# Kernel optimization log

Measured on AMD Instinct MI355X. Metric: run time of the kernel, lower is better.

## Reference

```python
import jax, jax.numpy as jnp
import numpy as np

N = 50000          # num nodes
NUM_HE = 10000     # num hyperedges
E = 800000         # num graph edges
INC = 800000       # num (node, hyperedge) incidences
IN_C, HID, OUT_C = 128, 128, 64
SLOPE = 0.01       # torch leaky_relu default negative slope


def _leaky(x):
    return jnp.where(x >= 0, x, SLOPE * x)


def hypergraph_conv(x, he_index, theta, bias):
    # PyG HypergraphConv (no attention, unit hyperedge weights):
    # out = D^{-1} H B^{-1} H^T (X Theta) + bias
    node_idx, he_idx = he_index[0], he_index[1]
    x = x @ theta                                            # [N, F]
    ones = jnp.ones(node_idx.shape[0], x.dtype)
    D = jax.ops.segment_sum(ones, node_idx, num_segments=N)           # node degree
    B = jax.ops.segment_sum(ones, he_idx, num_segments=NUM_HE)        # hyperedge degree
    Dinv = jnp.where(D > 0, 1.0 / D, 0.0)
    Binv = jnp.where(B > 0, 1.0 / B, 0.0)
    # node -> hyperedge
    m = jax.ops.segment_sum(x[node_idx], he_idx, num_segments=NUM_HE) * Binv[:, None]
    # hyperedge -> node
    out = jax.ops.segment_sum(m[he_idx], node_idx, num_segments=N) * Dinv[:, None]
    return out + bias


def graph_conv(x, edge_index, w_rel, b_rel, w_root):
    # PyG GraphConv (aggr='add'): out_i = W_rel * sum_{j->i} x_j + b_rel + W_root * x_i
    src, dst = edge_index[0], edge_index[1]
    agg = jax.ops.segment_sum(x[src], dst, num_segments=N)
    return agg @ w_rel + b_rel + x @ w_root


def _forward(X, edge_index, hyperedge_index,
             hc1_w, hc1_b, lin1_w, lin1_b,
             hc2_w, hc2_b, lin2_w, lin2_b,
             c1_wrel, c1_brel, c1_wroot, glin1_w, glin1_b,
             c2_wrel, c2_brel, c2_wroot, glin2_w, glin2_b,
             fc_w, fc_b):
    # dropout is identity in eval mode (and first two calls in the source discard their output)
    X = _leaky(hypergraph_conv(X, hyperedge_index, hc1_w, hc1_b) + (X @ lin1_w + lin1_b))
    X = _leaky(hypergraph_conv(X, hyperedge_index, hc2_w, hc2_b) + (X @ lin2_w + lin2_b))
    X = _leaky(graph_conv(X, edge_index, c1_wrel, c1_brel, c1_wroot) + (X @ glin1_w + glin1_b))
    X = _leaky(graph_conv(X, edge_index, c2_wrel, c2_brel, c2_wroot) + (X @ glin2_w + glin2_b))
    y = X @ fc_w + fc_b
    return X, y


def setup_inputs() -> dict:
    key = jax.random.key(0)
    ks = jax.random.split(key, 32)
    s = 0.02
    inp = {
        'X': jax.random.normal(ks[0], (N, IN_C), jnp.float32),
        'edge_index': jnp.stack([
            jax.random.randint(ks[1], (E,), 0, N),
            jax.random.randint(ks[2], (E,), 0, N)]).astype(jnp.int64),
        'hyperedge_index': jnp.stack([
            jax.random.randint(ks[3], (INC,), 0, N),
            jax.random.randint(ks[4], (INC,), 0, NUM_HE)]).astype(jnp.int64),
        'hc1_w': jax.random.normal(ks[5], (IN_C, HID), jnp.float32) * s,
        'hc1_b': jnp.zeros((HID,), jnp.float32),
        'lin1_w': jax.random.normal(ks[6], (IN_C, HID), jnp.float32) * s,
        'lin1_b': jnp.zeros((HID,), jnp.float32),
        'hc2_w': jax.random.normal(ks[7], (HID, HID), jnp.float32) * s,
        'hc2_b': jnp.zeros((HID,), jnp.float32),
        'lin2_w': jax.random.normal(ks[8], (HID, HID), jnp.float32) * s,
        'lin2_b': jnp.zeros((HID,), jnp.float32),
        'c1_wrel': jax.random.normal(ks[9], (HID, HID), jnp.float32) * s,
        'c1_brel': jnp.zeros((HID,), jnp.float32),
        'c1_wroot': jax.random.normal(ks[10], (HID, HID), jnp.float32) * s,
        'glin1_w': jax.random.normal(ks[11], (HID, HID), jnp.float32) * s,
        'glin1_b': jnp.zeros((HID,), jnp.float32),
        'c2_wrel': jax.random.normal(ks[12], (HID, HID), jnp.float32) * s,
        'c2_brel': jnp.zeros((HID,), jnp.float32),
        'c2_wroot': jax.random.normal(ks[13], (HID, HID), jnp.float32) * s,
        'glin2_w': jax.random.normal(ks[14], (HID, HID), jnp.float32) * s,
        'glin2_b': jnp.zeros((HID,), jnp.float32),
        'fc_w': jax.random.normal(ks[15], (HID, OUT_C), jnp.float32) * s,
        'fc_b': jnp.zeros((OUT_C,), jnp.float32),
    }
    return inp


def reference(X, edge_index, hyperedge_index,
              hc1_w, hc1_b, lin1_w, lin1_b,
              hc2_w, hc2_b, lin2_w, lin2_b,
              c1_wrel, c1_brel, c1_wroot, glin1_w, glin1_b,
              c2_wrel, c2_brel, c2_wroot, glin2_w, glin2_b,
              fc_w, fc_b):
    return _forward(X, edge_index, hyperedge_index,
                    hc1_w, hc1_b, lin1_w, lin1_b,
                    hc2_w, hc2_b, lin2_w, lin2_b,
                    c1_wrel, c1_brel, c1_wroot, glin1_w, glin1_b,
                    c2_wrel, c2_brel, c2_wroot, glin2_w, glin2_b,
                    fc_w, fc_b)
```

## Files before the change

### kernel.cpp

```cpp
#include <hip/hip_runtime.h>

#define NN 50000
#define HECNT 10000
#define EE 800000
#define II 800000
#define NBK 128
#define CHUNK 4096
#define BKCAP 8192

typedef _Float16 half8 __attribute__((ext_vector_type(8)));
typedef float f32x4    __attribute__((ext_vector_type(4)));
typedef unsigned short u16;

__device__ __forceinline__ int ld_idx(const int* p, long long pos, int is64) {
    return is64 ? p[pos * 2] : p[(int)pos];
}

__device__ __forceinline__ void task_info(int t, int& n, int& cbase, int& obase) {
    if (t == 0)      { n = HECNT; cbase = 0;           obase = 0; }
    else if (t == 1) { n = NN;    cbase = HECNT;       obase = HECNT + 1; }
    else             { n = NN;    cbase = HECNT + NN;  obase = HECNT + NN + 2; }
}

__device__ __forceinline__ void ld_edge(int t, long long i,
                                        const int* EIX, const int* HIX,
                                        int f0, int f1, int& d, int& v) {
    int rng;
    if (t == 0)      { d = ld_idx(HIX, (long long)II + i, f1); v = ld_idx(HIX, i, f1); rng = HECNT; }
    else if (t == 1) { d = ld_idx(HIX, i, f1); v = ld_idx(HIX, (long long)II + i, f1); rng = NN; }
    else             { d = ld_idx(EIX, (long long)EE + i, f0); v = ld_idx(EIX, i, f0); rng = NN; }
    if ((unsigned)d >= (unsigned)rng || (unsigned)v >= 65536u) d = -1;
}

__global__ void detect_binit_k(const int* __restrict__ EIX, const int* __restrict__ HIX,
                               int* __restrict__ flags, int* __restrict__ bcur) {
    int tid = threadIdx.x;
    int i = blockIdx.x * 256 + tid;
    if (i < 3 * NBK) bcur[i] = i * BKCAP;
    if (blockIdx.x == 0) {
        __shared__ int o0, o1;
        if (tid == 0) { o0 = 0; o1 = 0; }
        __syncthreads();
        atomicOr(&o0, EIX[2 * tid + 1]);
        atomicOr(&o1, HIX[2 * tid + 1]);
        __syncthreads();
        if (tid == 0) { flags[0] = (o0 == 0); flags[1] = (o1 == 0); }
    }
}

__global__ __launch_bounds__(256) void bin_k(const int* __restrict__ EIX,
                                             const int* __restrict__ HIX,
                                             const int* __restrict__ flags,
                                             int* __restrict__ bcur,
                                             unsigned* __restrict__ pairs) {
    int t = blockIdx.y;
    __shared__ int hcnt[NBK], hstart[NBK], hrun[NBK], gbase[NBK];
    __shared__ int stot;
    __shared__ unsigned stage[CHUNK];
    int tid = threadIdx.x;
    int n, cb, ob; task_info(t, n, cb, ob);
    int span = (n + NBK - 1) / NBK;
    long long base = (long long)blockIdx.x * CHUNK;
    int f0 = flags[0], f1 = flags[1];

    for (int i = tid; i < NBK; i += 256) { hcnt[i] = 0; hrun[i] = 0; }
    __syncthreads();

    int d[16], v[16];
    #pragma unroll
    for (int j = 0; j < 16; j++) {
        long long i = base + j * 256 + tid;
        int dd = -1, vv = 0;
        if (i < EE) ld_edge(t, i, EIX, HIX, f0, f1, dd, vv);
        d[j] = dd; v[j] = vv;
        if (dd >= 0) atomicAdd(&hcnt[dd / span], 1);
    }
    __syncthreads();

    if (tid < NBK) gbase[tid] = hcnt[tid] ? atomicAdd(&bcur[t * NBK + tid], hcnt[tid]) : 0;
    if (tid < NBK) hstart[tid] = hcnt[tid];
    __syncthreads();
    for (int o = 1; o < NBK; o <<= 1) {
        int u = 0;
        if (tid < NBK && tid >= o) u = hstart[tid - o];
        __syncthreads();
        if (tid < NBK) hstart[tid] += u;
        __syncthreads();
    }
    if (tid == NBK - 1) stot = hstart[tid];
    __syncthreads();
    if (tid < NBK) hstart[tid] -= hcnt[tid];
    __syncthreads();

    #pragma unroll
    for (int j = 0; j < 16; j++) {
        if (d[j] >= 0) {
            int b = d[j] / span;
            int p = hstart[b] + atomicAdd(&hrun[b], 1);
            stage[p] = ((unsigned)d[j] << 16) | (unsigned)v[j];
        }
    }
    __syncthreads();

    int total = stot;
    for (int i = tid; i < total; i += 256) {
        int lo = 0, hi = NBK - 1;
        while (lo < hi) { int mid = (lo + hi + 1) >> 1; if (hstart[mid] <= i) lo = mid; else hi = mid - 1; }
        int pos = gbase[lo] + (i - hstart[lo]);
        if (pos < (t * NBK + lo + 1) * BKCAP)
            pairs[pos] = stage[lo == 0 ? i : i];
    }
}

__global__ __launch_bounds__(384) void bscan_k(const int* __restrict__ bcur,
                                               int* __restrict__ bbase,
                                               int* __restrict__ offs) {
    __shared__ int sc[3 * NBK];
    int tid = threadIdx.x;
    int c = 0;
    if (tid < 3 * NBK) {
        c = bcur[tid] - tid * BKCAP;
        c = max(0, min(c, BKCAP));
        sc[tid] = c;
    }
    __syncthreads();
    int b = tid & (NBK - 1);
    for (int o = 1; o < NBK; o <<= 1) {
        int u = 0;
        if (tid < 3 * NBK && b >= o) u = sc[tid - o];
        __syncthreads();
        if (tid < 3 * NBK) sc[tid] += u;
        __syncthreads();
    }
    if (tid < 3 * NBK) {
        bbase[tid] = sc[tid] - c;
        if (b == NBK - 1) {
            int t = tid >> 7;
            int n, cb, ob; task_info(t, n, cb, ob);
            offs[ob + n] = sc[tid];
        }
    }
}

__global__ __launch_bounds__(256) void bfin_k(const int* __restrict__ bcur,
                                              const int* __restrict__ bbase,
                                              const unsigned* __restrict__ pairs,
                                              int* __restrict__ offs,
                                              u16* __restrict__ vals) {
    int idx = blockIdx.x;
    int t = idx / NBK, b = idx % NBK;
    int n, cb, ob; task_info(t, n, cb, ob);
    int span = (n + NBK - 1) / NBK;
    int dlo = min(b * span, n), dhi = min(dlo + span, n);
    if (dhi <= dlo) return;
    int nd = dhi - dlo;
    int cnt = bcur[idx] - idx * BKCAP;
    cnt = max(0, min(cnt, BKCAP));
    int base = bbase[idx];

    __shared__ int hist[512], sc[512], cur[400];
    __shared__ u16 win[BKCAP];
    int tid = threadIdx.x;
    for (int i = tid; i < 512; i += 256) { hist[i] = 0; }
    __syncthreads();

    const unsigned* pw = pairs + (size_t)idx * BKCAP;
    for (int i = tid; i < cnt; i += 256) {
        int dl = (int)(pw[i] >> 16) - dlo;
        if ((unsigned)dl < (unsigned)nd) atomicAdd(&hist[dl], 1);
    }
    __syncthreads();

    int s0 = tid, s1 = tid + 256;
    sc[s0] = hist[s0]; sc[s1] = hist[s1];
    __syncthreads();
    for (int o = 1; o < 512; o <<= 1) {
        int u0 = (s0 >= o) ? sc[s0 - o] : 0;
        int u1 = (s1 >= o) ? sc[s1 - o] : 0;
        __syncthreads();
        sc[s0] += u0; sc[s1] += u1;
        __syncthreads();
    }
    for (int i = tid; i < nd; i += 256) {
        int ex = sc[i] - hist[i];
        offs[ob + dlo + i] = base + ex;
        cur[i] = ex;
    }
    __syncthreads();

    for (int i = tid; i < cnt; i += 256) {
        unsigned pv = pw[i];
        int dl = (int)(pv >> 16) - dlo;
        if ((unsigned)dl < (unsigned)nd) {
            int p = atomicAdd(&cur[dl], 1);
            if ((unsigned)p < (unsigned)BKCAP) win[p] = (u16)(pv & 0xffffu);
        }
    }
    __syncthreads();
    u16* vw = vals + (size_t)t * 800000 + base;
    for (int i = tid; i < cnt; i += 256) vw[i] = win[i];
}

__global__ __launch_bounds__(256) void gather_k(const int* __restrict__ offs,
                                                const u16* __restrict__ vals,
                                                const _Float16* __restrict__ src,
                                                _Float16* __restrict__ out,
                                                int ndst, int nsrc, int scale_flag,
                                                const float* __restrict__ bias,
                                                const _Float16* __restrict__ addend,
                                                int act) {
    int wave = threadIdx.x >> 6, lane = threadIdx.x & 63;
    int sub = lane >> 4, l16 = lane & 15;
    int d = blockIdx.x * 4 + wave;
    if (d >= ndst) return;
    int beg = offs[d], end = offs[d + 1];
    int f = l16 * 8;
    float a[8] = {0.f, 0.f, 0.f, 0.f, 0.f, 0.f, 0.f, 0.f};
    auto acc_row = [&](int s) {
        if ((unsigned)s < (unsigned)nsrc) {
            half8 u = *(const half8*)(src + (size_t)s * 128 + f);
            #pragma unroll
            for (int j = 0; j < 8; j++) a[j] += (float)u[j];
        }
    };
    int e = beg + sub;
    for (; e + 12 < end; e += 16) {
        int s0 = vals[e], s1 = vals[e + 4], s2 = vals[e + 8], s3 = vals[e + 12];
        acc_row(s0); acc_row(s1); acc_row(s2); acc_row(s3);
    }
    for (; e < end; e += 4) acc_row(vals[e]);
    #pragma unroll
    for (int j = 0; j < 8; j++) {
        a[j] += __shfl_xor(a[j], 16, 64);
        a[j] += __shfl_xor(a[j], 32, 64);
    }
    if (sub == 0) {
        if (scale_flag) {
            int c = end - beg;
            float iv = (c > 0) ? 1.f / (float)c : 0.f;
            #pragma unroll
            for (int j = 0; j < 8; j++) a[j] *= iv;
        }
        if (bias) {
            f32x4 b0 = *(const f32x4*)(bias + f);
            f32x4 b1 = *(const f32x4*)(bias + f + 4);
            #pragma unroll
            for (int j = 0; j < 4; j++) { a[j] += b0[j]; a[4 + j] += b1[j]; }
        }
        if (addend) {
            half8 u = *(const half8*)(addend + (size_t)d * 128 + f);
            #pragma unroll
            for (int j = 0; j < 8; j++) a[j] += (float)u[j];
        }
        if (act) {
            #pragma unroll
            for (int j = 0; j < 8; j++) a[j] = (a[j] >= 0.f) ? a[j] : 0.01f * a[j];
        }
        half8 o;
        #pragma unroll
        for (int j = 0; j < 8; j++) o[j] = (_Float16)a[j];
        *(half8*)(out + (size_t)d * 128 + f) = o;
    }
}

__global__ __launch_bounds__(256) void wprep_k(const float* __restrict__ hc1_w, const float* __restrict__ lin1_w,
                                               const float* __restrict__ hc2_w, const float* __restrict__ lin2_w,
                                               const float* __restrict__ c1_wrel, const float* __restrict__ c1_wroot,
                                               const float* __restrict__ glin1_w,
                                               const float* __restrict__ c2_wrel, const float* __restrict__ c2_wroot,
                                               const float* __restrict__ glin2_w,
                                               const float* __restrict__ fc_w,
                                               _Float16* __restrict__ F) {
    int set = blockIdx.y;
    int nfrag = (set == 4) ? 1024 : 4096;
    int NT = (set < 2) ? 16 : (set == 4 ? 4 : 8);
    int fid = blockIdx.x * 256 + threadIdx.x;
    if (fid >= nfrag) return;
    int lane = fid & 63;
    int tile = fid >> 6;
    int nt = tile % NT, ks = tile / NT;
    int n = nt * 16 + (lane & 15);
    int kbase = ks * 32 + (lane >> 4) * 8;
    _Float16* dst = F + (size_t)set * 32768 + (size_t)fid * 8;
    #pragma unroll
    for (int j = 0; j < 8; j++) {
        int k = kbase + j;
        float w;
        if (set == 0)      w = (n < 128) ? hc1_w[k * 128 + n] : lin1_w[k * 128 + n - 128];
        else if (set == 1) w = (n < 128) ? hc2_w[k * 128 + n] : lin2_w[k * 128 + n - 128];
        else if (set == 2) w = (k < 128) ? c1_wrel[k * 128 + n]
                                         : c1_wroot[(k - 128) * 128 + n] + glin1_w[(k - 128) * 128 + n];
        else if (set == 3) w = (k < 128) ? c2_wrel[k * 128 + n]
                                         : c2_wroot[(k - 128) * 128 + n] + glin2_w[(k - 128) * 128 + n];
        else               w = fc_w[k * 64 + n];
        dst[j] = (_Float16)w;
    }
}

template <typename AT>
__global__ __launch_bounds__(256) void gemm2_k(const AT* __restrict__ A,
                                               const half8* __restrict__ Bf,
                                               const float* __restrict__ b2,
                                               _Float16* __restrict__ O1,
                                               _Float16* __restrict__ O2,
                                               int M) {
    constexpr int K = 128, NT = 16;
    int tid = threadIdx.x;
    int wave = tid >> 6, lane = tid & 63;
    int quad = lane >> 4, l16 = lane & 15;
    int rowbase = blockIdx.x * 64 + wave * 16;
    int row = rowbase + l16;

    f32x4 acc[NT];
    f32x4 zero4 = {0.f, 0.f, 0.f, 0.f};
    #pragma unroll
    for (int nt = 0; nt < NT; nt++) acc[nt] = zero4;

    #pragma unroll
    for (int ks = 0; ks < 4; ks++) {
        int k0 = ks * 32 + quad * 8;
        half8 af = {0, 0, 0, 0, 0, 0, 0, 0};
        if (row < M) {
            if constexpr (sizeof(AT) == 4) {
                const float* ap = (const float*)A + (size_t)row * K + k0;
                float4 x0 = *(const float4*)ap;
                float4 x1 = *(const float4*)(ap + 4);
                af = half8{(_Float16)x0.x, (_Float16)x0.y, (_Float16)x0.z, (_Float16)x0.w,
                           (_Float16)x1.x, (_Float16)x1.y, (_Float16)x1.z, (_Float16)x1.w};
            } else {
                af = *(const half8*)((const _Float16*)A + (size_t)row * K + k0);
            }
        }
        #pragma unroll
        for (int nt = 0; nt < NT; nt++) {
            half8 bfr = Bf[(ks * NT + nt) * 64 + lane];
            acc[nt] = __builtin_amdgcn_mfma_f32_16x16x32_f16(af, bfr, acc[nt], 0, 0, 0);
        }
    }

    #pragma unroll
    for (int nt = 0; nt < NT; nt++) {
        int col = nt * 16 + l16;
        bool second = (col >= 128);
        int c = second ? col - 128 : col;
        float bv = second ? b2[c] : 0.f;
        _Float16* O = second ? O2 : O1;
        #pragma unroll
        for (int r = 0; r < 4; r++) {
            int rr = rowbase + quad * 4 + r;
            if (rr < M) O[(size_t)rr * 128 + c] = (_Float16)(acc[nt][r] + bv);
        }
    }
}

__global__ __launch_bounds__(256) void gemmk2_k(const _Float16* __restrict__ A0,
                                                const _Float16* A1,
                                                const half8* __restrict__ Bf,
                                                const float* __restrict__ brel,
                                                const float* __restrict__ blin,
                                                float* __restrict__ Cf,
                                                _Float16* Ch,
                                                int M) {
    constexpr int NT = 8;
    int tid = threadIdx.x;
    int wave = tid >> 6, lane = tid & 63;
    int quad = lane >> 4, l16 = lane & 15;
    int rowbase = blockIdx.x * 64 + wave * 16;
    int row = rowbase + l16;

    f32x4 acc[NT];
    f32x4 zero4 = {0.f, 0.f, 0.f, 0.f};
    #pragma unroll
    for (int nt = 0; nt < NT; nt++) acc[nt] = zero4;

    #pragma unroll
    for (int ks = 0; ks < 8; ks++) {
        int k0 = ks * 32 + quad * 8;
        const _Float16* Asel = (k0 < 128) ? A0 : A1;
        int ka = k0 & 127;
        half8 af = {0, 0, 0, 0, 0, 0, 0, 0};
        if (row < M) af = *(const half8*)(Asel + (size_t)row * 128 + ka);
        #pragma unroll
        for (int nt = 0; nt < NT; nt++) {
            half8 bfr = Bf[(ks * NT + nt) * 64 + lane];
            acc[nt] = __builtin_amdgcn_mfma_f32_16x16x32_f16(af, bfr, acc[nt], 0, 0, 0);
        }
    }

    #pragma unroll
    for (int nt = 0; nt < NT; nt++) {
        int col = nt * 16 + l16;
        float bv = brel[col] + blin[col];
        #pragma unroll
        for (int r = 0; r < 4; r++) {
            int rr = rowbase + quad * 4 + r;
            if (rr < M) {
                float v = acc[nt][r] + bv;
                v = (v >= 0.f) ? v : 0.01f * v;
                if (Cf) Cf[(size_t)rr * 128 + col] = v;
                Ch[(size_t)rr * 128 + col] = (_Float16)v;
            }
        }
    }
}

__global__ __launch_bounds__(256) void gemmfc_k(const _Float16* __restrict__ A,
                                                const half8* __restrict__ Bf,
                                                const float* __restrict__ bias,
                                                float* __restrict__ C,
                                                int M) {
    constexpr int K = 128, N = 64, NT = 4;
    int tid = threadIdx.x;
    int wave = tid >> 6, lane = tid & 63;
    int quad = lane >> 4, l16 = lane & 15;
    int rowbase = blockIdx.x * 64 + wave * 16;
    int row = rowbase + l16;

    f32x4 acc[NT];
    f32x4 zero4 = {0.f, 0.f, 0.f, 0.f};
    #pragma unroll
    for (int nt = 0; nt < NT; nt++) acc[nt] = zero4;

    #pragma unroll
    for (int ks = 0; ks < 4; ks++) {
        int k0 = ks * 32 + quad * 8;
        half8 af = {0, 0, 0, 0, 0, 0, 0, 0};
        if (row < M) af = *(const half8*)(A + (size_t)row * K + k0);
        #pragma unroll
        for (int nt = 0; nt < NT; nt++) {
            half8 bfr = Bf[(ks * NT + nt) * 64 + lane];
            acc[nt] = __builtin_amdgcn_mfma_f32_16x16x32_f16(af, bfr, acc[nt], 0, 0, 0);
        }
    }

    #pragma unroll
    for (int nt = 0; nt < NT; nt++) {
        int col = nt * 16 + l16;
        float bv = bias[col];
        #pragma unroll
        for (int r = 0; r < 4; r++) {
            int rr = rowbase + quad * 4 + r;
            if (rr < M) C[(size_t)rr * N + col] = acc[nt][r] + bv;
        }
    }
}

extern "C" void kernel_launch(void* const* d_in, const int* in_sizes, int n_in,
                              void* d_out, int out_size, void* d_ws, size_t ws_size,
                              hipStream_t stream) {
    const float* X       = (const float*)d_in[0];
    const int*   EIX     = (const int*)d_in[1];
    const int*   HIX     = (const int*)d_in[2];
    const float* hc1_w   = (const float*)d_in[3];
    const float* hc1_b   = (const float*)d_in[4];
    const float* lin1_w  = (const float*)d_in[5];
    const float* lin1_b  = (const float*)d_in[6];
    const float* hc2_w   = (const float*)d_in[7];
    const float* hc2_b   = (const float*)d_in[8];
    const float* lin2_w  = (const float*)d_in[9];
    const float* lin2_b  = (const float*)d_in[10];
    const float* c1_wrel = (const float*)d_in[11];
    const float* c1_brel = (const float*)d_in[12];
    const float* c1_wroot= (const float*)d_in[13];
    const float* glin1_w = (const float*)d_in[14];
    const float* glin1_b = (const float*)d_in[15];
    const float* c2_wrel = (const float*)d_in[16];
    const float* c2_brel = (const float*)d_in[17];
    const float* c2_wroot= (const float*)d_in[18];
    const float* glin2_w = (const float*)d_in[19];
    const float* glin2_b = (const float*)d_in[20];
    const float* fc_w    = (const float*)d_in[21];
    const float* fc_b    = (const float*)d_in[22];

    char* wsp = (char*)d_ws;
    size_t off = 0;
    auto carve = [&](size_t bytes) -> char* {
        char* p = wsp + off;
        off = (off + bytes + 255) & ~(size_t)255;
        return p;
    };
    int*   flags  = (int*)carve(16);
    int*   offs   = (int*)carve(110003 * 4);
    int*   bcur   = (int*)carve(3 * NBK * 4);
    int*   bbase  = (int*)carve(3 * NBK * 4);
    u16*   vals   = (u16*)carve(2400000 * 2);
    _Float16* F   = (_Float16*)carve((4 * 32768 + 8192) * 2);
    char*  U      = carve((size_t)NN * 128 * 2 * 2);
    _Float16* P  = (_Float16*)U;
    _Float16* L  = (_Float16*)(U + (size_t)NN * 128 * 2);
    unsigned* pairs = (unsigned*)U;
    _Float16* MH = (_Float16*)carve((size_t)HECNT * 128 * 2);
    _Float16* XA = (_Float16*)carve((size_t)NN * 128 * 2);

    float* XO = (float*)d_out;
    float* YO = XO + (size_t)NN * 128;

    const half8* F0 = (const half8*)F;
    const half8* F1 = (const half8*)(F + 32768);
    const half8* F2 = (const half8*)(F + 2 * 32768);
    const half8* F3 = (const half8*)(F + 3 * 32768);
    const half8* F4 = (const half8*)(F + 4 * 32768);

    detect_binit_k<<<2, 256, 0, stream>>>(EIX, HIX, flags, bcur);
    wprep_k<<<dim3(16, 5), 256, 0, stream>>>(hc1_w, lin1_w, hc2_w, lin2_w,
                                             c1_wrel, c1_wroot, glin1_w,
                                             c2_wrel, c2_wroot, glin2_w, fc_w, F);
    bin_k<<<dim3((EE + CHUNK - 1) / CHUNK, 3), 256, 0, stream>>>(EIX, HIX, flags, bcur, pairs);
    bscan_k<<<1, 384, 0, stream>>>(bcur, bbase, offs);
    bfin_k<<<3 * NBK, 256, 0, stream>>>(bcur, bbase, pairs, offs, vals);

    const int* offs_he   = offs;
    const int* offs_node = offs + HECNT + 1;
    const int* offs_dst  = offs + HECNT + NN + 2;
    const u16* vals_he   = vals;
    const u16* vals_node = vals + 800000;
    const u16* vals_dst  = vals + 1600000;

    int g64 = (NN + 63) / 64;
    int ghe = (HECNT + 3) / 4;
    int gnn = (NN + 3) / 4;

    gemm2_k<float><<<g64, 256, 0, stream>>>(X, F0, lin1_b, P, L, NN);
    gather_k<<<ghe, 256, 0, stream>>>(offs_he, vals_he, P, MH, HECNT, NN, 1, nullptr, nullptr, 0);
    gather_k<<<gnn, 256, 0, stream>>>(offs_node, vals_node, MH, XA, NN, HECNT, 1, hc1_b, L, 1);

    gemm2_k<_Float16><<<g64, 256, 0, stream>>>(XA, F1, lin2_b, P, L, NN);
    gather_k<<<ghe, 256, 0, stream>>>(offs_he, vals_he, P, MH, HECNT, NN, 1, nullptr, nullptr, 0);
    gather_k<<<gnn, 256, 0, stream>>>(offs_node, vals_node, MH, XA, NN, HECNT, 1, hc2_b, L, 1);

    gather_k<<<gnn, 256, 0, stream>>>(offs_dst, vals_dst, XA, P, NN, NN, 0, nullptr, nullptr, 0);
    gemmk2_k<<<g64, 256, 0, stream>>>(P, XA, F2, c1_brel, glin1_b, nullptr, XA, NN);

    gather_k<<<gnn, 256, 0, stream>>>(offs_dst, vals_dst, XA, P, NN, NN, 0, nullptr, nullptr, 0);
    gemmk2_k<<<g64, 256, 0, stream>>>(P, XA, F3, c2_brel, glin2_b, XO, XA, NN);

    gemmfc_k<<<g64, 256, 0, stream>>>(XA, F4, fc_b, YO, NN);
}
```

Measured before the change: 477.2 us.

## Fuse preprocessing, binning with first GEMM, and gathers into GEMM kernels

Merges the flag/bucket init into the weight-prep kernel, runs edge binning and the first projection GEMM in one launch, and folds the bucket scan into the finalize kernel. Gathers feeding GEMMs now write into LDS tiles consumed directly by MFMA, and the final FC GEMM is fused into the last graph-conv kernel. Binning loads are vectorized and the gather loop is unrolled deeper. This cuts launch count and intermediate HBM round-trips, but per-block gather work in the fused kernels is serialized over 16 rows per wave, which may lower parallelism.

Result: slower. 531.2 us (+11.3%).

```diff
diff --git a/kernel.cpp b/kernel.cpp
--- a/kernel.cpp
+++ b/kernel.cpp
@@ -7,14 +7,11 @@
 #define NBK 128
 #define CHUNK 4096
 #define BKCAP 8192
+#define BIN_GRID ((EE + CHUNK - 1) / CHUNK)
 
 typedef _Float16 half8 __attribute__((ext_vector_type(8)));
 typedef float f32x4    __attribute__((ext_vector_type(4)));
 typedef unsigned short u16;
-
-__device__ __forceinline__ int ld_idx(const int* p, long long pos, int is64) {
-    return is64 ? p[pos * 2] : p[(int)pos];
-}
 
 __device__ __forceinline__ void task_info(int t, int& n, int& cbase, int& obase) {
     if (t == 0)      { n = HECNT; cbase = 0;           obase = 0; }
@@ -22,22 +19,21 @@
     else             { n = NN;    cbase = HECNT + NN;  obase = HECNT + NN + 2; }
 }
 
-__device__ __forceinline__ void ld_edge(int t, long long i,
-                                        const int* EIX, const int* HIX,
-                                        int f0, int f1, int& d, int& v) {
-    int rng;
-    if (t == 0)      { d = ld_idx(HIX, (long long)II + i, f1); v = ld_idx(HIX, i, f1); rng = HECNT; }
-    else if (t == 1) { d = ld_idx(HIX, i, f1); v = ld_idx(HIX, (long long)II + i, f1); rng = NN; }
-    else             { d = ld_idx(EIX, (long long)EE + i, f0); v = ld_idx(EIX, i, f0); rng = NN; }
-    if ((unsigned)d >= (unsigned)rng || (unsigned)v >= 65536u) d = -1;
-}
-
-__global__ void detect_binit_k(const int* __restrict__ EIX, const int* __restrict__ HIX,
-                               int* __restrict__ flags, int* __restrict__ bcur) {
+__global__ __launch_bounds__(256) void prep_k(const int* __restrict__ EIX, const int* __restrict__ HIX,
+                                              int* __restrict__ flags, int* __restrict__ bcur,
+                                              const float* __restrict__ hc1_w, const float* __restrict__ lin1_w,
+                                              const float* __restrict__ hc2_w, const float* __restrict__ lin2_w,
+                                              const float* __restrict__ c1_wrel, const float* __restrict__ c1_wroot,
+                                              const float* __restrict__ glin1_w,
+                                              const float* __restrict__ c2_wrel, const float* __restrict__ c2_wroot,
+                                              const float* __restrict__ glin2_w,
+                                              const float* __restrict__ fc_w,
+                                              _Float16* __restrict__ F) {
+    int set = blockIdx.y;
     int tid = threadIdx.x;
-    int i = blockIdx.x * 256 + tid;
-    if (i < 3 * NBK) bcur[i] = i * BKCAP;
-    if (blockIdx.x == 0) {
+    if (set == 5) {
+        if (blockIdx.x != 0) return;
+        for (int i = tid; i < 3 * NBK; i += 256) bcur[i] = i * BKCAP;
         __shared__ int o0, o1;
         if (tid == 0) { o0 = 0; o1 = 0; }
         __syncthreads();
@@ -45,35 +41,77 @@
         atomicOr(&o1, HIX[2 * tid + 1]);
         __syncthreads();
         if (tid == 0) { flags[0] = (o0 == 0); flags[1] = (o1 == 0); }
-    }
-}
-
-__global__ __launch_bounds__(256) void bin_k(const int* __restrict__ EIX,
-                                             const int* __restrict__ HIX,
-                                             const int* __restrict__ flags,
-                                             int* __restrict__ bcur,
-                                             unsigned* __restrict__ pairs) {
-    int t = blockIdx.y;
+        return;
+    }
+    int nfrag = (set == 4) ? 1024 : 4096;
+    int NT = (set < 2) ? 16 : (set == 4 ? 4 : 8);
+    int fid = blockIdx.x * 256 + tid;
+    if (fid >= nfrag) return;
+    int lane = fid & 63;
+    int tile = fid >> 6;
+    int nt = tile % NT, ks = tile / NT;
+    int n = nt * 16 + (lane & 15);
+    int kbase = ks * 32 + (lane >> 4) * 8;
+    _Float16* dst = F + (size_t)set * 32768 + (size_t)fid * 8;
+    #pragma unroll
+    for (int j = 0; j < 8; j++) {
+        int k = kbase + j;
+        float w;
+        if (set == 0)      w = (n < 128) ? hc1_w[k * 128 + n] : lin1_w[k * 128 + n - 128];
+        else if (set == 1) w = (n < 128) ? hc2_w[k * 128 + n] : lin2_w[k * 128 + n - 128];
+        else if (set == 2) w = (k < 128) ? c1_wrel[k * 128 + n]
+                                         : c1_wroot[(k - 128) * 128 + n] + glin1_w[(k - 128) * 128 + n];
+        else if (set == 3) w = (k < 128) ? c2_wrel[k * 128 + n]
+                                         : c2_wroot[(k - 128) * 128 + n] + glin2_w[(k - 128) * 128 + n];
+        else               w = fc_w[k * 64 + n];
+        dst[j] = (_Float16)w;
+    }
+}
+
+__device__ void bin_body(int bx, int t,
+                         const int* __restrict__ EIX, const int* __restrict__ HIX,
+                         const int* __restrict__ flags, int* __restrict__ bcur,
+                         unsigned* __restrict__ pairs) {
     __shared__ int hcnt[NBK], hstart[NBK], hrun[NBK], gbase[NBK];
     __shared__ int stot;
     __shared__ unsigned stage[CHUNK];
     int tid = threadIdx.x;
     int n, cb, ob; task_info(t, n, cb, ob);
     int span = (n + NBK - 1) / NBK;
-    long long base = (long long)blockIdx.x * CHUNK;
-    int f0 = flags[0], f1 = flags[1];
+    long long base = (long long)bx * CHUNK;
+    int f = (t == 2) ? flags[0] : flags[1];
+    const int* arr = (t == 2) ? EIX : HIX;
+    int mul = f ? 2 : 1;
+    const int* row1 = arr + (size_t)mul * 800000;
+    const int* darr = (t == 1) ? arr : row1;
+    const int* varr = (t == 1) ? row1 : arr;
+    int rng = (t == 0) ? HECNT : NN;
 
     for (int i = tid; i < NBK; i += 256) { hcnt[i] = 0; hrun[i] = 0; }
     __syncthreads();
 
     int d[16], v[16];
     #pragma unroll
-    for (int j = 0; j < 16; j++) {
-        long long i = base + j * 256 + tid;
-        int dd = -1, vv = 0;
-        if (i < EE) ld_edge(t, i, EIX, HIX, f0, f1, dd, vv);
-        d[j] = dd; v[j] = vv;
-        if (dd >= 0) atomicAdd(&hcnt[dd / span], 1);
+    for (int jj = 0; jj < 8; jj++) {
+        long long i = base + jj * 512 + tid * 2;
+        int d0 = -1, d1 = -1, v0 = 0, v1 = 0;
+        if (i < EE) {
+            if (f) {
+                int4 dw = *(const int4*)(darr + 2 * i);
+                int4 vw = *(const int4*)(varr + 2 * i);
+                d0 = dw.x; d1 = dw.z; v0 = vw.x; v1 = vw.z;
+            } else {
+                int2 dw = *(const int2*)(darr + i);
+                int2 vw = *(const int2*)(varr + i);
+                d0 = dw.x; d1 = dw.y; v0 = vw.x; v1 = vw.y;
+            }
+            if ((unsigned)d0 >= (unsigned)rng || (unsigned)v0 >= 65536u) d0 = -1;
+            if ((unsigned)d1 >= (unsigned)rng || (unsigned)v1 >= 65536u) d1 = -1;
+        }
+        d[2 * jj] = d0; v[2 * jj] = v0;
+        d[2 * jj + 1] = d1; v[2 * jj + 1] = v1;
+        if (d0 >= 0) atomicAdd(&hcnt[d0 / span], 1);
+        if (d1 >= 0) atomicAdd(&hcnt[d1 / span], 1);
     }
     __syncthreads();
 
@@ -108,59 +146,105 @@
         while (lo < hi) { int mid = (lo + hi + 1) >> 1; if (hstart[mid] <= i) lo = mid; else hi = mid - 1; }
         int pos = gbase[lo] + (i - hstart[lo]);
         if (pos < (t * NBK + lo + 1) * BKCAP)
-            pairs[pos] = stage[lo == 0 ? i : i];
-    }
-}
-
-__global__ __launch_bounds__(384) void bscan_k(const int* __restrict__ bcur,
-                                               int* __restrict__ bbase,
-                                               int* __restrict__ offs) {
-    __shared__ int sc[3 * NBK];
+            pairs[pos] = stage[i];
+    }
+}
+
+__device__ void gemm2_f32(int bx, const float* __restrict__ A,
+                          const half8* __restrict__ Bf,
+                          const float* __restrict__ b2,
+                          _Float16* __restrict__ O1, _Float16* __restrict__ O2, int M) {
+    constexpr int K = 128, NT = 16;
     int tid = threadIdx.x;
-    int c = 0;
-    if (tid < 3 * NBK) {
-        c = bcur[tid] - tid * BKCAP;
-        c = max(0, min(c, BKCAP));
-        sc[tid] = c;
-    }
-    __syncthreads();
-    int b = tid & (NBK - 1);
-    for (int o = 1; o < NBK; o <<= 1) {
-        int u = 0;
-        if (tid < 3 * NBK && b >= o) u = sc[tid - o];
-        __syncthreads();
-        if (tid < 3 * NBK) sc[tid] += u;
-        __syncthreads();
-    }
-    if (tid < 3 * NBK) {
-        bbase[tid] = sc[tid] - c;
-        if (b == NBK - 1) {
-            int t = tid >> 7;
-            int n, cb, ob; task_info(t, n, cb, ob);
-            offs[ob + n] = sc[tid];
-        }
-    }
-}
-
-__global__ __launch_bounds__(256) void bfin_k(const int* __restrict__ bcur,
-                                              const int* __restrict__ bbase,
-                                              const unsigned* __restrict__ pairs,
-                                              int* __restrict__ offs,
-                                              u16* __restrict__ vals) {
+    int wave = tid >> 6, lane = tid & 63;
+    int quad = lane >> 4, l16 = lane & 15;
+    int rowbase = bx * 64 + wave * 16;
+    int row = rowbase + l16;
+
+    f32x4 acc[NT];
+    f32x4 zero4 = {0.f, 0.f, 0.f, 0.f};
+    #pragma unroll
+    for (int nt = 0; nt < NT; nt++) acc[nt] = zero4;
+
+    #pragma unroll
+    for (int ks = 0; ks < 4; ks++) {
+        int k0 = ks * 32 + quad * 8;
+        half8 af = {0, 0, 0, 0, 0, 0, 0, 0};
+        if (row < M) {
+            const float* ap = A + (size_t)row * K + k0;
+            float4 x0 = *(const float4*)ap;
+            float4 x1 = *(const float4*)(ap + 4);
+            af = half8{(_Float16)x0.x, (_Float16)x0.y, (_Float16)x0.z, (_Float16)x0.w,
+                       (_Float16)x1.x, (_Float16)x1.y, (_Float16)x1.z, (_Float16)x1.w};
+        }
+        #pragma unroll
+        for (int nt = 0; nt < NT; nt++) {
+            half8 bfr = Bf[(ks * NT + nt) * 64 + lane];
+            acc[nt] = __builtin_amdgcn_mfma_f32_16x16x32_f16(af, bfr, acc[nt], 0, 0, 0);
+        }
+    }
+
+    #pragma unroll
+    for (int nt = 0; nt < NT; nt++) {
+        int col = nt * 16 + l16;
+        bool second = (col >= 128);
+        int c = second ? col - 128 : col;
+        float bv = second ? b2[c] : 0.f;
+        _Float16* O = second ? O2 : O1;
+        #pragma unroll
+        for (int r = 0; r < 4; r++) {
+            int rr = rowbase + quad * 4 + r;
+            if (rr < M) O[(size_t)rr * 128 + c] = (_Float16)(acc[nt][r] + bv);
+        }
+    }
+}
+
+__global__ __launch_bounds__(256) void phase1_k(const int* __restrict__ EIX, const int* __restrict__ HIX,
+                                                const int* __restrict__ flags, int* __restrict__ bcur,
+                                                unsigned* __restrict__ pairs,
+                                                const float* __restrict__ X, const half8* __restrict__ F0,
+                                                const float* __restrict__ lin1_b,
+                                                _Float16* __restrict__ P, _Float16* __restrict__ L) {
+    int bx = blockIdx.x;
+    if (bx < 3 * BIN_GRID) {
+        bin_body(bx % BIN_GRID, bx / BIN_GRID, EIX, HIX, flags, bcur, pairs);
+    } else {
+        gemm2_f32(bx - 3 * BIN_GRID, X, F0, lin1_b, P, L, NN);
+    }
+}
+
+__global__ __launch_bounds__(256) void bfin2_k(const int* __restrict__ bcur,
+                                               const unsigned* __restrict__ pairs,
+                                               int* __restrict__ offs,
+                                               u16* __restrict__ vals) {
     int idx = blockIdx.x;
     int t = idx / NBK, b = idx % NBK;
     int n, cb, ob; task_info(t, n, cb, ob);
     int span = (n + NBK - 1) / NBK;
     int dlo = min(b * span, n), dhi = min(dlo + span, n);
+    int tid = threadIdx.x;
+
+    __shared__ int scnt[NBK];
+    if (tid < NBK) {
+        int c = bcur[t * NBK + tid] - (t * NBK + tid) * BKCAP;
+        scnt[tid] = max(0, min(c, BKCAP));
+    }
+    __syncthreads();
+    for (int o = 1; o < NBK; o <<= 1) {
+        int u = 0;
+        if (tid < NBK && tid >= o) u = scnt[tid - o];
+        __syncthreads();
+        if (tid < NBK) scnt[tid] += u;
+        __syncthreads();
+    }
+    if (b == NBK - 1 && tid == 0) offs[ob + n] = scnt[NBK - 1];
     if (dhi <= dlo) return;
     int nd = dhi - dlo;
-    int cnt = bcur[idx] - idx * BKCAP;
-    cnt = max(0, min(cnt, BKCAP));
-    int base = bbase[idx];
+    int base = (b > 0) ? scnt[b - 1] : 0;
+    int cnt = scnt[b] - base;
 
     __shared__ int hist[512], sc[512], cur[400];
     __shared__ u16 win[BKCAP];
-    int tid = threadIdx.x;
     for (int i = tid; i < 512; i += 256) { hist[i] = 0; }
     __syncthreads();
 
@@ -224,6 +308,12 @@
         }
     };
     int e = beg + sub;
+    for (; e + 28 < end; e += 32) {
+        int s0 = vals[e], s1 = vals[e + 4], s2 = vals[e + 8], s3 = vals[e + 12];
+        int s4 = vals[e + 16], s5 = vals[e + 20], s6 = vals[e + 24], s7 = vals[e + 28];
+        acc_row(s0); acc_row(s1); acc_row(s2); acc_row(s3);
+        acc_row(s4); acc_row(s5); acc_row(s6); acc_row(s7);
+    }
     for (; e + 12 < end; e += 16) {
         int s0 = vals[e], s1 = vals[e + 4], s2 = vals[e + 8], s3 = vals[e + 12];
         acc_row(s0); acc_row(s1); acc_row(s2); acc_row(s3);
@@ -263,53 +353,87 @@
     }
 }
 
-__global__ __launch_bounds__(256) void wprep_k(const float* __restrict__ hc1_w, const float* __restrict__ lin1_w,
-                                               const float* __restrict__ hc2_w, const float* __restrict__ lin2_w,
-                                               const float* __restrict__ c1_wrel, const float* __restrict__ c1_wroot,
-                                               const float* __restrict__ glin1_w,
-                                               const float* __restrict__ c2_wrel, const float* __restrict__ c2_wroot,
-                                               const float* __restrict__ glin2_w,
-                                               const float* __restrict__ fc_w,
-                                               _Float16* __restrict__ F) {
-    int set = blockIdx.y;
-    int nfrag = (set == 4) ? 1024 : 4096;
-    int NT = (set < 2) ? 16 : (set == 4 ? 4 : 8);
-    int fid = blockIdx.x * 256 + threadIdx.x;
-    if (fid >= nfrag) return;
-    int lane = fid & 63;
-    int tile = fid >> 6;
-    int nt = tile % NT, ks = tile / NT;
-    int n = nt * 16 + (lane & 15);
-    int kbase = ks * 32 + (lane >> 4) * 8;
-    _Float16* dst = F + (size_t)set * 32768 + (size_t)fid * 8;
-    #pragma unroll
-    for (int j = 0; j < 8; j++) {
-        int k = kbase + j;
-        float w;
-        if (set == 0)      w = (n < 128) ? hc1_w[k * 128 + n] : lin1_w[k * 128 + n - 128];
-        else if (set == 1) w = (n < 128) ? hc2_w[k * 128 + n] : lin2_w[k * 128 + n - 128];
-        else if (set == 2) w = (k < 128) ? c1_wrel[k * 128 + n]
-                                         : c1_wroot[(k - 128) * 128 + n] + glin1_w[(k - 128) * 128 + n];
-        else if (set == 3) w = (k < 128) ? c2_wrel[k * 128 + n]
-                                         : c2_wroot[(k - 128) * 128 + n] + glin2_w[(k - 128) * 128 + n];
-        else               w = fc_w[k * 64 + n];
-        dst[j] = (_Float16)w;
-    }
-}
-
-template <typename AT>
-__global__ __launch_bounds__(256) void gemm2_k(const AT* __restrict__ A,
-                                               const half8* __restrict__ Bf,
-                                               const float* __restrict__ b2,
-                                               _Float16* __restrict__ O1,
-                                               _Float16* __restrict__ O2,
-                                               int M) {
-    constexpr int K = 128, NT = 16;
+__device__ __forceinline__ void gather_to_lds(_Float16* lt,
+        const int* __restrict__ offs, const u16* __restrict__ vals,
+        const _Float16* __restrict__ src,
+        int row0, int ndst, int nsrc, int scale_flag,
+        const float* __restrict__ bias, const _Float16* __restrict__ addend, int act) {
+    int wave = threadIdx.x >> 6, lane = threadIdx.x & 63;
+    int sub = lane >> 4, l16 = lane & 15;
+    int f = l16 * 8;
+    int oi = min(row0 + wave * 16 + lane, ndst);
+    int ov = (lane <= 16) ? offs[oi] : 0;
+    for (int i = 0; i < 16; i++) {
+        int dl = wave * 16 + i;
+        int d = row0 + dl;
+        int beg = __shfl(ov, i, 64);
+        int end = __shfl(ov, i + 1, 64);
+        float a[8] = {0.f, 0.f, 0.f, 0.f, 0.f, 0.f, 0.f, 0.f};
+        auto acc_row = [&](int s) {
+            if ((unsigned)s < (unsigned)nsrc) {
+                half8 u = *(const half8*)(src + (size_t)s * 128 + f);
+                #pragma unroll
+                for (int j = 0; j < 8; j++) a[j] += (float)u[j];
+            }
+        };
+        int e = beg + sub;
+        for (; e + 28 < end; e += 32) {
+            int s0 = vals[e], s1 = vals[e + 4], s2 = vals[e + 8], s3 = vals[e + 12];
+            int s4 = vals[e + 16], s5 = vals[e + 20], s6 = vals[e + 24], s7 = vals[e + 28];
+            acc_row(s0); acc_row(s1); acc_row(s2); acc_row(s3);
+            acc_row(s4); acc_row(s5); acc_row(s6); acc_row(s7);
+        }
+        for (; e + 12 < end; e += 16) {
+            int s0 = vals[e], s1 = vals[e + 4], s2 = vals[e + 8], s3 = vals[e + 12];
+            acc_row(s0); acc_row(s1); acc_row(s2); acc_row(s3);
+        }
+        for (; e < end; e += 4) acc_row(vals[e]);
+        #pragma unroll
+        for (int j = 0; j < 8; j++) {
+            a[j] += __shfl_xor(a[j], 16, 64);
+            a[j] += __shfl_xor(a[j], 32, 64);
+        }
+        if (sub == 0) {
+            if (d < ndst) {
+                if (scale_flag) {
+                    int c = end - beg;
+                    float iv = (c > 0) ? 1.f / (float)c : 0.f;
+                    #pragma unroll
+                    for (int j = 0; j < 8; j++) a[j] *= iv;
+                }
+                if (bias) {
+                    f32x4 b0 = *(const f32x4*)(bias + f);
+                    f32x4 b1 = *(const f32x4*)(bias + f + 4);
+                    #pragma unroll
+                    for (int j = 0; j < 4; j++) { a[j] += b0[j]; a[4 + j] += b1[j]; }
+                }
+                if (addend) {
+                    half8 u = *(const half8*)(addend + (size_t)d * 128 + f);
+                    #pragma unroll
+                    for (int j = 0; j < 8; j++) a[j] += (float)u[j];
+                }
+                if (act) {
+                    #pragma unroll
+                    for (int j = 0; j < 8; j++) a[j] = (a[j] >= 0.f) ? a[j] : 0.01f * a[j];
+                }
+            }
+            half8 o;
+            #pragma unroll
+            for (int j = 0; j < 8; j++) o[j] = (_Float16)a[j];
+            *(half8*)(lt + dl * 136 + f) = o;
+        }
+    }
+}
+
+__device__ __forceinline__ void gemm2_lds(const _Float16* lt, const half8* __restrict__ Bf,
+                                          const float* __restrict__ b2,
+                                          _Float16* __restrict__ O1, _Float16* __restrict__ O2,
+                                          int rowblk, int M) {
+    constexpr int NT = 16;
     int tid = threadIdx.x;
     int wave = tid >> 6, lane = tid & 63;
     int quad = lane >> 4, l16 = lane & 15;
-    int rowbase = blockIdx.x * 64 + wave * 16;
-    int row = rowbase + l16;
+    int rowbase = rowblk + wave * 16;
 
     f32x4 acc[NT];
     f32x4 zero4 = {0.f, 0.f, 0.f, 0.f};
@@ -319,18 +443,7 @@
     #pragma unroll
     for (int ks = 0; ks < 4; ks++) {
         int k0 = ks * 32 + quad * 8;
-        half8 af = {0, 0, 0, 0, 0, 0, 0, 0};
-        if (row < M) {
-            if constexpr (sizeof(AT) == 4) {
-                const float* ap = (const float*)A + (size_t)row * K + k0;
-                float4 x0 = *(const float4*)ap;
-                float4 x1 = *(const float4*)(ap + 4);
-                af = half8{(_Float16)x0.x, (_Float16)x0.y, (_Float16)x0.z, (_Float16)x0.w,
-                           (_Float16)x1.x, (_Float16)x1.y, (_Float16)x1.z, (_Float16)x1.w};
-            } else {
-                af = *(const half8*)((const _Float16*)A + (size_t)row * K + k0);
-            }
-        }
+        half8 af = *(const half8*)(lt + (wave * 16 + l16) * 136 + k0);
         #pragma unroll
         for (int nt = 0; nt < NT; nt++) {
             half8 bfr = Bf[(ks * NT + nt) * 64 + lane];
@@ -353,19 +466,46 @@
     }
 }
 
-__global__ __launch_bounds__(256) void gemmk2_k(const _Float16* __restrict__ A0,
-                                                const _Float16* A1,
-                                                const half8* __restrict__ Bf,
-                                                const float* __restrict__ brel,
-                                                const float* __restrict__ blin,
-                                                float* __restrict__ Cf,
-                                                _Float16* Ch,
-                                                int M) {
+__global__ __launch_bounds__(256) void gatherN_gemm2_k(const int* __restrict__ offs,
+                                                       const u16* __restrict__ vals,
+                                                       const _Float16* __restrict__ MH,
+                                                       const float* __restrict__ bias,
+                                                       const _Float16* __restrict__ addend,
+                                                       const half8* __restrict__ Bf,
+                                                       const float* __restrict__ b2,
+                                                       _Float16* __restrict__ O1,
+                                                       _Float16* __restrict__ O2,
+                                                       int M) {
+    __shared__ __align__(16) _Float16 lt[64 * 136];
+    int rowblk = blockIdx.x * 64;
+    gather_to_lds(lt, offs, vals, MH, rowblk, M, HECNT, 1, bias, addend, 1);
+    __syncthreads();
+    gemm2_lds(lt, Bf, b2, O1, O2, rowblk, M);
+}
+
+template <int FC>
+__global__ __launch_bounds__(256) void gconv_k(const int* __restrict__ offs,
+                                               const u16* __restrict__ vals,
+                                               const _Float16* __restrict__ Xin,
+                                               const half8* __restrict__ Bf,
+                                               const float* __restrict__ brel,
+                                               const float* __restrict__ blin,
+                                               float* __restrict__ Cf,
+                                               _Float16* __restrict__ Ch,
+                                               const half8* __restrict__ Bfc,
+                                               const float* __restrict__ bfc,
+                                               float* __restrict__ Y,
+                                               int M) {
+    __shared__ __align__(16) _Float16 lt[64 * 136];
+    int rowblk = blockIdx.x * 64;
+    gather_to_lds(lt, offs, vals, Xin, rowblk, M, M, 0, nullptr, nullptr, 0);
+    __syncthreads();
+
     constexpr int NT = 8;
     int tid = threadIdx.x;
     int wave = tid >> 6, lane = tid & 63;
     int quad = lane >> 4, l16 = lane & 15;
-    int rowbase = blockIdx.x * 64 + wave * 16;
+    int rowbase = rowblk + wave * 16;
     int row = rowbase + l16;
 
     f32x4 acc[NT];
@@ -376,10 +516,12 @@
     #pragma unroll
     for (int ks = 0; ks < 8; ks++) {
         int k0 = ks * 32 + quad * 8;
-        const _Float16* Asel = (k0 < 128) ? A0 : A1;
-        int ka = k0 & 127;
         half8 af = {0, 0, 0, 0, 0, 0, 0, 0};
-        if (row < M) af = *(const half8*)(Asel + (size_t)row * 128 + ka);
+        if (ks < 4) {
+            af = *(const half8*)(lt + (wave * 16 + l16) * 136 + k0);
+        } else if (row < M) {
+            af = *(const half8*)(Xin + (size_t)row * 128 + (k0 - 128));
+        }
         #pragma unroll
         for (int nt = 0; nt < NT; nt++) {
             half8 bfr = Bf[(ks * NT + nt) * 64 + lane];
@@ -394,53 +536,38 @@
         #pragma unroll
         for (int r = 0; r < 4; r++) {
             int rr = rowbase + quad * 4 + r;
+            float v = acc[nt][r] + bv;
+            v = (v >= 0.f) ? v : 0.01f * v;
             if (rr < M) {
-                float v = acc[nt][r] + bv;
-                v = (v >= 0.f) ? v : 0.01f * v;
-                if (Cf) Cf[(size_t)rr * 128 + col] = v;
-                Ch[(size_t)rr * 128 + col] = (_Float16)v;
+                if (FC) Cf[(size_t)rr * 128 + col] = v;
+                else    Ch[(size_t)rr * 128 + col] = (_Float16)v;
             }
-        }
-    }
-}
-
-__global__ __launch_bounds__(256) void gemmfc_k(const _Float16* __restrict__ A,
-                                                const half8* __restrict__ Bf,
-                                                const float* __restrict__ bias,
-                                                float* __restrict__ C,
-                                                int M) {
-    constexpr int K = 128, N = 64, NT = 4;
-    int tid = threadIdx.x;
-    int wave = tid >> 6, lane = tid & 63;
-    int quad = lane >> 4, l16 = lane & 15;
-    int rowbase = blockIdx.x * 64 + wave * 16;
-    int row = rowbase + l16;
-
-    f32x4 acc[NT];
-    f32x4 zero4 = {0.f, 0.f, 0.f, 0.f};
-    #pragma unroll
-    for (int nt = 0; nt < NT; nt++) acc[nt] = zero4;
-
-    #pragma unroll
-    for (int ks = 0; ks < 4; ks++) {
-        int k0 = ks * 32 + quad * 8;
-        half8 af = {0, 0, 0, 0, 0, 0, 0, 0};
-        if (row < M) af = *(const half8*)(A + (size_t)row * K + k0);
-        #pragma unroll
-        for (int nt = 0; nt < NT; nt++) {
-            half8 bfr = Bf[(ks * NT + nt) * 64 + lane];
-            acc[nt] = __builtin_amdgcn_mfma_f32_16x16x32_f16(af, bfr, acc[nt], 0, 0, 0);
-        }
-    }
-
-    #pragma unroll
-    for (int nt = 0; nt < NT; nt++) {
-        int col = nt * 16 + l16;
-        float bv = bias[col];
-        #pragma unroll
-        for (int r = 0; r < 4; r++) {
-            int rr = rowbase + quad * 4 + r;
-            if (rr < M) C[(size_t)rr * N + col] = acc[nt][r] + bv;
+            if (FC) lt[(wave * 16 + quad * 4 + r) * 136 + col] = (_Float16)v;
+        }
+    }
+
+    if (FC) {
+        f32x4 a2[4];
+        #pragma unroll
+        for (int nt = 0; nt < 4; nt++) a2[nt] = zero4;
+        #pragma unroll
+        for (int ks = 0; ks < 4; ks++) {
+            half8 af = *(const half8*)(lt + (wave * 16 + l16) * 136 + ks * 32 + quad * 8);
+            #pragma unroll
+            for (int nt = 0; nt < 4; nt++) {
+                half8 bfr = Bfc[(ks * 4 + nt) * 64 + lane];
+                a2[nt] = __builtin_amdgcn_mfma_f32_16x16x32_f16(af, bfr, a2[nt], 0, 0, 0);
+            }
+        }
+        #pragma unroll
+        for (int nt = 0; nt < 4; nt++) {
+            int col = nt * 16 + l16;
+            float bv = bfc[col];
+            #pragma unroll
+            for (int r = 0; r < 4; r++) {
+                int rr = rowbase + quad * 4 + r;
+                if (rr < M) Y[(size_t)rr * 64 + col] = a2[nt][r] + bv;
+            }
         }
     }
 }
@@ -482,15 +609,14 @@
     int*   flags  = (int*)carve(16);
     int*   offs   = (int*)carve(110003 * 4);
     int*   bcur   = (int*)carve(3 * NBK * 4);
-    int*   bbase  = (int*)carve(3 * NBK * 4);
     u16*   vals   = (u16*)carve(2400000 * 2);
     _Float16* F   = (_Float16*)carve((4 * 32768 + 8192) * 2);
-    char*  U      = carve((size_t)NN * 128 * 2 * 2);
-    _Float16* P  = (_Float16*)U;
-    _Float16* L  = (_Float16*)(U + (size_t)NN * 128 * 2);
-    unsigned* pairs = (unsigned*)U;
+    unsigned* pairs = (unsigned*)carve((size_t)3 * NBK * BKCAP * 4);
+    _Float16* P  = (_Float16*)carve((size_t)NN * 128 * 2);
+    _Float16* L  = (_Float16*)carve((size_t)NN * 128 * 2);
     _Float16* MH = (_Float16*)carve((size_t)HECNT * 128 * 2);
     _Float16* XA = (_Float16*)carve((size_t)NN * 128 * 2);
+    _Float16* XB = P;
 
     float* XO = (float*)d_out;
     float* YO = XO + (size_t)NN * 128;
@@ -500,14 +626,6 @@
     const half8* F2 = (const half8*)(F + 2 * 32768);
     const half8* F3 = (const half8*)(F + 3 * 32768);
     const half8* F4 = (const half8*)(F + 4 * 32768);
-
-    detect_binit_k<<<2, 256, 0, stream>>>(EIX, HIX, flags, bcur);
-    wprep_k<<<dim3(16, 5), 256, 0, stream>>>(hc1_w, lin1_w, hc2_w, lin2_w,
-                                             c1_wrel, c1_wroot, glin1_w,
-                                             c2_wrel, c2_wroot, glin2_w, fc_w, F);
-    bin_k<<<dim3((EE + CHUNK - 1) / CHUNK, 3), 256, 0, stream>>>(EIX, HIX, flags, bcur, pairs);
-    bscan_k<<<1, 384, 0, stream>>>(bcur, bbase, offs);
-    bfin_k<<<3 * NBK, 256, 0, stream>>>(bcur, bbase, pairs, offs, vals);
 
     const int* offs_he   = offs;
     const int* offs_node = offs + HECNT + 1;
@@ -520,19 +638,22 @@
     int ghe = (HECNT + 3) / 4;
     int gnn = (NN + 3) / 4;
 
-    gemm2_k<float><<<g64, 256, 0, stream>>>(X, F0, lin1_b, P, L, NN);
+    prep_k<<<dim3(16, 6), 256, 0, stream>>>(EIX, HIX, flags, bcur,
+                                            hc1_w, lin1_w, hc2_w, lin2_w,
+                                            c1_wrel, c1_wroot, glin1_w,
+                                            c2_wrel, c2_wroot, glin2_w, fc_w, F);
+    phase1_k<<<3 * BIN_GRID + g64, 256, 0, stream>>>(EIX, HIX, flags, bcur, pairs,
+                                                     X, F0, lin1_b, P, L);
+    bfin2_k<<<3 * NBK, 256, 0, stream>>>(bcur, pairs, offs, vals);
+
     gather_k<<<ghe, 256, 0, stream>>>(offs_he, vals_he, P, MH, HECNT, NN, 1, nullptr, nullptr, 0);
-    gather_k<<<gnn, 256, 0, stream>>>(offs_node, vals_node, MH, XA, NN, HECNT, 1, hc1_b, L, 1);
-
-    gemm2_k<_Float16><<<g64, 256, 0, stream>>>(XA, F1, lin2_b, P, L, NN);
+    gatherN_gemm2_k<<<g64, 256, 0, stream>>>(offs_node, vals_node, MH, hc1_b, L,
+                                             F1, lin2_b, P, L, NN);
     gather_k<<<ghe, 256, 0, stream>>>(offs_he, vals_he, P, MH, HECNT, NN, 1, nullptr, nullptr, 0);
     gather_k<<<gnn, 256, 0, stream>>>(offs_node, vals_node, MH, XA, NN, HECNT, 1, hc2_b, L, 1);
 
-    gather_k<<<gnn, 256, 0, stream>>>(offs_dst, vals_dst, XA, P, NN, NN, 0, nullptr, nullptr, 0);
-    gemmk2_k<<<g64, 256, 0, stream>>>(P, XA, F2, c1_brel, glin1_b, nullptr, XA, NN);
-
-    gather_k<<<gnn, 256, 0, stream>>>(offs_dst, vals_dst, XA, P, NN, NN, 0, nullptr, nullptr, 0);
-    gemmk2_k<<<g64, 256, 0, stream>>>(P, XA, F3, c2_brel, glin2_b, XO, XA, NN);
-
-    gemmfc_k<<<g64, 256, 0, stream>>>(XA, F4, fc_b, YO, NN);
-}
+    gconv_k<0><<<g64, 256, 0, stream>>>(offs_dst, vals_dst, XA, F2, c1_brel, glin1_b,
+                                        nullptr, XB, nullptr, nullptr, nullptr, NN);
+    gconv_k<1><<<g64, 256, 0, stream>>>(offs_dst, vals_dst, XB, F3, c2_brel, glin2_b,
+                                        XO, nullptr, F4, fc_b, YO, NN);
+}
```
